# Kernel tuning notes

Hardware: AMD Instinct MI355X
Metric: run time of the kernel (lower is better)

The kernel has to match this reference:

```python
import jax, jax.numpy as jnp
import numpy as np

H = 16      # num_head
D = 1024    # feat_dim
DK = D // H # per-head dim
B, S = 2, 2048


def setup_inputs() -> dict:
    key = jax.random.key(0)
    ks = jax.random.split(key, 11)
    scale = 1.0 / np.sqrt(D)
    inp = {
        'query': jax.random.normal(ks[0], (B, S, D), jnp.float32),
        'key':   jax.random.normal(ks[1], (B, S, D), jnp.float32),
        'value': jax.random.normal(ks[2], (B, S, D), jnp.float32),
        # causal lower-triangular mask (seq, seq); 0 entries get -1e9
        'mask':  jnp.tril(jnp.ones((S, S), jnp.int32)),
        # torch nn.Linear params: y = x @ W.T + b
        'w_q': jax.random.normal(ks[3], (D, D), jnp.float32) * scale,
        'b_q': jax.random.normal(ks[4], (D,), jnp.float32) * scale,
        'w_k': jax.random.normal(ks[5], (D, D), jnp.float32) * scale,
        'b_k': jax.random.normal(ks[6], (D,), jnp.float32) * scale,
        'w_v': jax.random.normal(ks[7], (D, D), jnp.float32) * scale,
        'b_v': jax.random.normal(ks[8], (D,), jnp.float32) * scale,
        'w_out': jax.random.normal(ks[9], (D, D), jnp.float32) * scale,
        'b_out': jax.random.normal(ks[10], (D,), jnp.float32) * scale,
    }
    return inp


def reference(query, key, value, mask, w_q, b_q, w_k, b_k, w_v, b_v, w_out, b_out):
    b = query.shape[0]
    # projections + split heads -> (b, h, s, d_k)
    def proj(x, w, bias):
        y = x @ w.T + bias
        return y.reshape(b, -1, H, DK).transpose(0, 2, 1, 3)
    q = proj(query, w_q, b_q)
    k = proj(key, w_k, b_k)
    v = proj(value, w_v, b_v)
    # scaled dot-product attention with materialized score matrix
    scores = jnp.einsum('bhqd,bhkd->bhqk', q, k) / np.sqrt(DK).astype(jnp.float32)
    scores = jnp.where(mask == 0, jnp.float32(-1e9), scores)
    attn = jax.nn.softmax(scores, axis=-1)  # dropout is identity in eval mode
    x = jnp.einsum('bhqk,bhkd->bhqd', attn, v)
    x = x.transpose(0, 2, 1, 3).reshape(b, -1, H * DK)
    return x @ w_out.T + b_out
```

## Files before the change

### kernel.cpp

```cpp
#include <hip/hip_runtime.h>

typedef unsigned short u16;
typedef __attribute__((ext_vector_type(8))) short short8;
typedef __attribute__((ext_vector_type(8))) unsigned short u16x8;
typedef __attribute__((ext_vector_type(4))) float floatx4;

#define S2LOG 0.18033688f

__device__ __forceinline__ u16 f2bf(float f) {
    unsigned int u = __float_as_uint(f);
    return (u16)((u + 0x7FFFu + ((u >> 16) & 1u)) >> 16);
}
__device__ __forceinline__ u16 f2bf_hu(float f) {
    return (u16)((__float_as_uint(f) + 0x8000u) >> 16);
}
__device__ __forceinline__ void gl_lds16(const u16* g, u16* l) {
    __builtin_amdgcn_global_load_lds(
        (const __attribute__((address_space(1))) void*)g,
        (__attribute__((address_space(3))) void*)l, 16, 0, 0);
}

__global__ __launch_bounds__(256) void cvt_all(
    const float* __restrict__ q, const float* __restrict__ k, const float* __restrict__ v,
    const float* __restrict__ wq, const float* __restrict__ wk,
    const float* __restrict__ wv, const float* __restrict__ wo,
    u16* __restrict__ ws)
{
    const int b = blockIdx.x, t = threadIdx.x;
    const float* src; u16* dst; long blk;
    if      (b < 2048) { src = q;  dst = ws;            blk = b; }
    else if (b < 4096) { src = k;  dst = ws + 4194304;  blk = b - 2048; }
    else if (b < 6144) { src = v;  dst = ws + 8388608;  blk = b - 4096; }
    else if (b < 6656) { src = wq; dst = ws + 12582912; blk = b - 6144; }
    else if (b < 7168) { src = wk; dst = ws + 13631488; blk = b - 6656; }
    else if (b < 7680) { src = wv; dst = ws + 14680064; blk = b - 7168; }
    else               { src = wo; dst = ws + 15728640; blk = b - 7680; }
    const long i = blk * 2048 + (long)t * 8;
    const float4 a = *(const float4*)(src + i);
    const float4 c = *(const float4*)(src + i + 4);
    u16x8 o;
    o[0] = f2bf(a.x); o[1] = f2bf(a.y); o[2] = f2bf(a.z); o[3] = f2bf(a.w);
    o[4] = f2bf(c.x); o[5] = f2bf(c.y); o[6] = f2bf(c.z); o[7] = f2bf(c.w);
    *(u16x8*)(dst + i) = o;
}

__device__ __forceinline__ void gemm_core64(
    const u16* __restrict__ A, const u16* __restrict__ Bw,
    int m0, int n0, floatx4 (&acc)[2][4])
{
    __shared__ u16 As[2][128 * 64];
    __shared__ u16 Bs[2][64 * 64];
    const int t = threadIdx.x, w = t >> 6;
    const int lane = t & 63, col = lane & 15, quad = lane >> 4;
    const int c7 = col & 7;

#pragma unroll
    for (int i = 0; i < 2; ++i)
#pragma unroll
        for (int j = 0; j < 4; ++j) acc[i][j] = (floatx4)0.f;

    auto stage = [&](int k0, int buf) {
#pragma unroll
        for (int jj = 0; jj < 4; ++jj) {
            const int c = jj * 256 + t;
            const int row = c >> 3, kc = (c & 7) ^ (row & 7);
            gl_lds16(A + (size_t)(m0 + row) * 1024 + k0 + kc * 8,
                     As[buf] + (jj * 256 + w * 64) * 8);
        }
#pragma unroll
        for (int jj = 0; jj < 2; ++jj) {
            const int c = jj * 256 + t;
            const int row = c >> 3, kc = (c & 7) ^ (row & 7);
            gl_lds16(Bw + (size_t)(n0 + row) * 1024 + k0 + kc * 8,
                     Bs[buf] + (jj * 256 + w * 64) * 8);
        }
    };

    stage(0, 0);
    int cur = 0;
    for (int k0 = 0; k0 < 1024; k0 += 64) {
        asm volatile("s_waitcnt vmcnt(0)" ::: "memory");
        __builtin_amdgcn_s_barrier();
        if (k0 + 64 < 1024) stage(k0 + 64, cur ^ 1);
#pragma unroll
        for (int ks = 0; ks < 2; ++ks) {
            const int swz = (ks * 4 + quad) ^ c7;
            short8 af[2], bf[4];
#pragma unroll
            for (int i = 0; i < 2; ++i)
                af[i] = *(const short8*)&As[cur][((w * 32 + i * 16 + col) * 8 + swz) * 8];
#pragma unroll
            for (int j = 0; j < 4; ++j)
                bf[j] = *(const short8*)&Bs[cur][((j * 16 + col) * 8 + swz) * 8];
#pragma unroll
            for (int i = 0; i < 2; ++i)
#pragma unroll
                for (int j = 0; j < 4; ++j)
                    acc[i][j] = __builtin_amdgcn_mfma_f32_16x16x32_bf16(
                        af[i], bf[j], acc[i][j], 0, 0, 0);
        }
        asm volatile("s_waitcnt lgkmcnt(0)" ::: "memory");
        cur ^= 1;
    }
}

__device__ __forceinline__ void gemm_core128(
    const u16* __restrict__ A, const u16* __restrict__ Bw,
    int m0, int n0, floatx4 (&acc)[4][4])
{
    __shared__ u16 As[2][128 * 64];
    __shared__ u16 Bs[2][128 * 64];
    const int t = threadIdx.x, w = t >> 6;
    const int lane = t & 63, col = lane & 15, quad = lane >> 4;
    const int c7 = col & 7;
    const int wr = (w >> 1) * 64, wc = (w & 1) * 64;

#pragma unroll
    for (int i = 0; i < 4; ++i)
#pragma unroll
        for (int j = 0; j < 4; ++j) acc[i][j] = (floatx4)0.f;

    auto stage = [&](int k0, int buf) {
#pragma unroll
        for (int jj = 0; jj < 4; ++jj) {
            const int c = jj * 256 + t;
            const int row = c >> 3, kc = (c & 7) ^ (row & 7);
            gl_lds16(A + (size_t)(m0 + row) * 1024 + k0 + kc * 8,
                     As[buf] + (jj * 256 + w * 64) * 8);
            gl_lds16(Bw + (size_t)(n0 + row) * 1024 + k0 + kc * 8,
                     Bs[buf] + (jj * 256 + w * 64) * 8);
        }
    };

    stage(0, 0);
    int cur = 0;
    for (int k0 = 0; k0 < 1024; k0 += 64) {
        asm volatile("s_waitcnt vmcnt(0)" ::: "memory");
        __builtin_amdgcn_s_barrier();
        if (k0 + 64 < 1024) stage(k0 + 64, cur ^ 1);
#pragma unroll
        for (int ks = 0; ks < 2; ++ks) {
            const int swz = (ks * 4 + quad) ^ c7;
            short8 af[4], bf[4];
#pragma unroll
            for (int i = 0; i < 4; ++i)
                af[i] = *(const short8*)&As[cur][((wr + i * 16 + col) * 8 + swz) * 8];
#pragma unroll
            for (int j = 0; j < 4; ++j)
                bf[j] = *(const short8*)&Bs[cur][((wc + j * 16 + col) * 8 + swz) * 8];
#pragma unroll
            for (int i = 0; i < 4; ++i)
#pragma unroll
                for (int j = 0; j < 4; ++j)
                    acc[i][j] = __builtin_amdgcn_mfma_f32_16x16x32_bf16(
                        af[i], bf[j], acc[i][j], 0, 0, 0);
        }
        asm volatile("s_waitcnt lgkmcnt(0)" ::: "memory");
        cur ^= 1;
    }
}

__global__ __launch_bounds__(256) void gemm_qkv(
    const u16* __restrict__ xq, const u16* __restrict__ xk, const u16* __restrict__ xv,
    const u16* __restrict__ wqb, const u16* __restrict__ wkb, const u16* __restrict__ wvb,
    const float* __restrict__ bq, const float* __restrict__ bk, const float* __restrict__ bv,
    u16* __restrict__ Qh, u16* __restrict__ Kh, u16* __restrict__ Vt)
{
    const int z = blockIdx.z;
    const u16*   A    = z == 0 ? xq  : z == 1 ? xk  : xv;
    const u16*   Bw   = z == 0 ? wqb : z == 1 ? wkb : wvb;
    const float* bias = z == 0 ? bq  : z == 1 ? bk  : bv;
    u16*         out  = z == 0 ? Qh  : z == 1 ? Kh  : Vt;
    const float  scale = z == 0 ? S2LOG : 1.0f;
    const int m0 = blockIdx.x * 128, n0 = blockIdx.y * 128;

    floatx4 acc[4][4];
    gemm_core128(A, Bw, m0, n0, acc);

    const int t = threadIdx.x, w = t >> 6;
    const int lane = t & 63, col = lane & 15, quad = lane >> 4;
    const int wr = (w >> 1) * 64, wc = (w & 1) * 64;
#pragma unroll
    for (int i = 0; i < 4; ++i)
#pragma unroll
        for (int j = 0; j < 4; ++j)
#pragma unroll
            for (int reg = 0; reg < 4; ++reg) {
                const int gm = m0 + wr + i * 16 + quad * 4 + reg;
                const int gn = n0 + wc + j * 16 + col;
                const float val = (acc[i][j][reg] + bias[gn]) * scale;
                const int bb = gm >> 11, ss = gm & 2047, hh = gn >> 6, dd = gn & 63;
                if (z != 2)
                    out[(((size_t)bb * 16 + hh) * 2048 + ss) * 64 + dd] = f2bf(val);
                else
                    out[(((size_t)bb * 16 + hh) * 64 + dd) * 2048 + ss] = f2bf(val);
            }
}

__global__ __launch_bounds__(256) void gemm_out(
    const u16* __restrict__ A, const u16* __restrict__ Bw,
    const float* __restrict__ bias, float* __restrict__ out)
{
    const int m0 = blockIdx.x * 128, n0 = blockIdx.y * 64;
    floatx4 acc[2][4];
    gemm_core64(A, Bw, m0, n0, acc);
    const int t = threadIdx.x, w = t >> 6;
    const int lane = t & 63, col = lane & 15, quad = lane >> 4;
#pragma unroll
    for (int i = 0; i < 2; ++i)
#pragma unroll
        for (int j = 0; j < 4; ++j)
#pragma unroll
            for (int reg = 0; reg < 4; ++reg) {
                const int gm = m0 + w * 32 + i * 16 + quad * 4 + reg;
                const int gn = n0 + j * 16 + col;
                out[(size_t)gm * 1024 + gn] = acc[i][j][reg] + bias[gn];
            }
}

__global__ __launch_bounds__(256) void attn_mfma(
    const u16* __restrict__ Qh, const u16* __restrict__ Kh,
    const u16* __restrict__ Vt, u16* __restrict__ ctx)
{
    __shared__ u16 QPs[64 * 64];
    __shared__ u16 Ks[2][64 * 64];
    __shared__ u16 Vs[2][64 * 64];
    const int t = threadIdx.x, w = t >> 6;
    const int lane = t & 63, col = lane & 15, quad = lane >> 4;
    const int c7 = col & 7;
    const int bh = blockIdx.y;
    const int qt = (bh < 16) ? (31 - (int)blockIdx.x) : (int)blockIdx.x;
    const int q0 = qt * 64;
    const u16* qg = Qh + ((size_t)bh * 2048 + q0) * 64;
    const u16* kg = Kh + (size_t)bh * 2048 * 64;
    const u16* vg = Vt + (size_t)bh * 2048 * 64;

    auto stage = [&](int tile, int buf) {
#pragma unroll
        for (int jj = 0; jj < 2; ++jj) {
            const int c = jj * 256 + t;
            const int row = c >> 3, kc = (c & 7) ^ (row & 7);
            gl_lds16(kg + (size_t)(tile * 64 + row) * 64 + kc * 8,
                     Ks[buf] + (jj * 256 + w * 64) * 8);
            gl_lds16(vg + (size_t)row * 2048 + tile * 64 + kc * 8,
                     Vs[buf] + (jj * 256 + w * 64) * 8);
        }
    };

#pragma unroll
    for (int jj = 0; jj < 2; ++jj) {
        const int c = jj * 256 + t;
        const int row = c >> 3, kc = (c & 7) ^ (row & 7);
        gl_lds16(qg + (size_t)row * 64 + kc * 8, QPs + (jj * 256 + w * 64) * 8);
    }
    stage(0, 0);
    asm volatile("s_waitcnt vmcnt(4)" ::: "memory");
    __builtin_amdgcn_s_barrier();

    short8 qf[2];
#pragma unroll
    for (int ks = 0; ks < 2; ++ks)
        qf[ks] = *(const short8*)
            &QPs[((w * 16 + col) * 8 + ((ks * 4 + quad) ^ c7)) * 8];
    asm volatile("s_waitcnt lgkmcnt(0)" ::: "memory");
    __builtin_amdgcn_s_barrier();

    floatx4 oacc[4], lacc;
    lacc = (floatx4)0.f;
#pragma unroll
    for (int j = 0; j < 4; ++j) oacc[j] = (floatx4)0.f;
    short8 ones;
#pragma unroll
    for (int i = 0; i < 8; ++i) ones[i] = (short)0x3F80;

    const int ktmax = qt;
    int cur = 0;
    for (int kt = 0; kt <= ktmax; ++kt) {
        asm volatile("s_waitcnt vmcnt(0)" ::: "memory");
        __builtin_amdgcn_s_barrier();
        if (kt + 1 <= ktmax) stage(kt + 1, cur ^ 1);

        floatx4 sa[4];
#pragma unroll
        for (int j = 0; j < 4; ++j) sa[j] = (floatx4)0.f;
#pragma unroll
        for (int ks = 0; ks < 2; ++ks) {
            const int swz = (ks * 4 + quad) ^ c7;
            short8 kf[4];
#pragma unroll
            for (int jc = 0; jc < 4; ++jc)
                kf[jc] = *(const short8*)&Ks[cur][((jc * 16 + col) * 8 + swz) * 8];
            __builtin_amdgcn_s_setprio(1);
#pragma unroll
            for (int jc = 0; jc < 4; ++jc)
                sa[jc] = __builtin_amdgcn_mfma_f32_16x16x32_bf16(
                    qf[ks], kf[jc], sa[jc], 0, 0, 0);
            __builtin_amdgcn_s_setprio(0);
        }
        const bool pm = (kt == qt);
#pragma unroll
        for (int reg = 0; reg < 4; ++reg) {
            const int prow = w * 16 + quad * 4 + reg;
            const int qrow = q0 + prow;
            const int pr7 = prow & 7;
            u16* pr = &QPs[prow * 64 + (col & 7)];
#pragma unroll
            for (int jc = 0; jc < 4; ++jc) {
                float p = __builtin_amdgcn_exp2f(sa[jc][reg]);
                if (pm && (kt * 64 + jc * 16 + col > qrow)) p = 0.f;
                pr[((2 * jc + (col >> 3)) ^ pr7) << 3] = f2bf_hu(p);
            }
        }
#pragma unroll
        for (int ks = 0; ks < 2; ++ks) {
            const int swz = (ks * 4 + quad) ^ c7;
            short8 pf, vf[4];
            pf = *(const short8*)&QPs[((w * 16 + col) * 8 + swz) * 8];
#pragma unroll
            for (int jd = 0; jd < 4; ++jd)
                vf[jd] = *(const short8*)&Vs[cur][((jd * 16 + col) * 8 + swz) * 8];
            __builtin_amdgcn_s_setprio(1);
            lacc = __builtin_amdgcn_mfma_f32_16x16x32_bf16(pf, ones, lacc, 0, 0, 0);
#pragma unroll
            for (int jd = 0; jd < 4; ++jd)
                oacc[jd] = __builtin_amdgcn_mfma_f32_16x16x32_bf16(
                    pf, vf[jd], oacc[jd], 0, 0, 0);
            __builtin_amdgcn_s_setprio(0);
        }
        cur ^= 1;
    }

    const int bb = bh >> 4, hh = bh & 15;
#pragma unroll
    for (int reg = 0; reg < 4; ++reg) {
        const float inv = __builtin_amdgcn_rcpf(lacc[reg]);
        const int qrow = q0 + w * 16 + quad * 4 + reg;
#pragma unroll
        for (int jd = 0; jd < 4; ++jd)
            ctx[((size_t)bb * 2048 + qrow) * 1024 + hh * 64 + jd * 16 + col] =
                f2bf(oacc[jd][reg] * inv);
    }
}

extern "C" void kernel_launch(void* const* d_in, const int* in_sizes, int n_in,
                              void* d_out, int out_size, void* d_ws, size_t ws_size,
                              hipStream_t stream)
{
    const float* query = (const float*)d_in[0];
    const float* key   = (const float*)d_in[1];
    const float* value = (const float*)d_in[2];
    const float* w_q   = (const float*)d_in[4];
    const float* b_q   = (const float*)d_in[5];
    const float* w_k   = (const float*)d_in[6];
    const float* b_k   = (const float*)d_in[7];
    const float* w_v   = (const float*)d_in[8];
    const float* b_v   = (const float*)d_in[9];
    const float* w_out = (const float*)d_in[10];
    const float* b_out = (const float*)d_in[11];

    u16* W = (u16*)d_ws;
    u16* xq  = W;
    u16* xk  = W + 4194304;
    u16* xv  = W + 8388608;
    u16* wqb = W + 12582912;
    u16* wkb = W + 13631488;
    u16* wvb = W + 14680064;
    u16* wob = W + 15728640;
    u16* Qh  = W + 16777216;
    u16* Kh  = W + 20971520;
    u16* Vtw = W + 25165824;
    u16* ctx = W + 29360128;

    hipLaunchKernelGGL(cvt_all, dim3(8192), dim3(256), 0, stream,
                       query, key, value, w_q, w_k, w_v, w_out, W);

    hipLaunchKernelGGL(gemm_qkv, dim3(32, 8, 3), dim3(256), 0, stream,
                       xq, xk, xv, wqb, wkb, wvb, b_q, b_k, b_v, Qh, Kh, Vtw);

    hipLaunchKernelGGL(attn_mfma, dim3(32, 32), dim3(256), 0, stream, Qh, Kh, Vtw, ctx);

    hipLaunchKernelGGL(gemm_out, dim3(32, 16), dim3(256), 0, stream,
                       ctx, wob, b_out, (float*)d_out);
}
```

Measured before the change: 244.7 us.

## Load K/V MFMA fragments directly from global memory instead of LDS staging

The attention kernel no longer stages Q, K and V tiles through double-buffered LDS with async global-to-LDS copies and barriers. Each wave now reads its MFMA operand fragments straight from global memory (relying on L2/L1 reuse across waves), and LDS is kept only for the P tile. The intent is to remove barriers and LDS traffic and shrink the LDS footprint, and launch bounds now ask for 3 blocks per CU for more occupancy. The cost is four-fold redundant global loads across the waves, no explicit prefetch of the next tile, and exposed load latency inside the loop.

Result: slower. 333.7 us (+36.4%).

```diff
diff --git a/kernel.cpp b/kernel.cpp
--- a/kernel.cpp
+++ b/kernel.cpp
@@ -218,13 +218,11 @@
             }
 }
 
-__global__ __launch_bounds__(256) void attn_mfma(
+__global__ __launch_bounds__(256, 3) void attn_mfma(
     const u16* __restrict__ Qh, const u16* __restrict__ Kh,
     const u16* __restrict__ Vt, u16* __restrict__ ctx)
 {
-    __shared__ u16 QPs[64 * 64];
-    __shared__ u16 Ks[2][64 * 64];
-    __shared__ u16 Vs[2][64 * 64];
+    __shared__ u16 Ps[64 * 64];
     const int t = threadIdx.x, w = t >> 6;
     const int lane = t & 63, col = lane & 15, quad = lane >> 4;
     const int c7 = col & 7;
@@ -235,35 +233,10 @@
     const u16* kg = Kh + (size_t)bh * 2048 * 64;
     const u16* vg = Vt + (size_t)bh * 2048 * 64;
 
-    auto stage = [&](int tile, int buf) {
-#pragma unroll
-        for (int jj = 0; jj < 2; ++jj) {
-            const int c = jj * 256 + t;
-            const int row = c >> 3, kc = (c & 7) ^ (row & 7);
-            gl_lds16(kg + (size_t)(tile * 64 + row) * 64 + kc * 8,
-                     Ks[buf] + (jj * 256 + w * 64) * 8);
-            gl_lds16(vg + (size_t)row * 2048 + tile * 64 + kc * 8,
-                     Vs[buf] + (jj * 256 + w * 64) * 8);
-        }
-    };
-
-#pragma unroll
-    for (int jj = 0; jj < 2; ++jj) {
-        const int c = jj * 256 + t;
-        const int row = c >> 3, kc = (c & 7) ^ (row & 7);
-        gl_lds16(qg + (size_t)row * 64 + kc * 8, QPs + (jj * 256 + w * 64) * 8);
-    }
-    stage(0, 0);
-    asm volatile("s_waitcnt vmcnt(4)" ::: "memory");
-    __builtin_amdgcn_s_barrier();
-
     short8 qf[2];
 #pragma unroll
     for (int ks = 0; ks < 2; ++ks)
-        qf[ks] = *(const short8*)
-            &QPs[((w * 16 + col) * 8 + ((ks * 4 + quad) ^ c7)) * 8];
-    asm volatile("s_waitcnt lgkmcnt(0)" ::: "memory");
-    __builtin_amdgcn_s_barrier();
+        qf[ks] = *(const short8*)(qg + (size_t)(w * 16 + col) * 64 + (ks * 4 + quad) * 8);
 
     floatx4 oacc[4], lacc;
     lacc = (floatx4)0.f;
@@ -273,37 +246,44 @@
 #pragma unroll
     for (int i = 0; i < 8; ++i) ones[i] = (short)0x3F80;
 
+    const u16* kb = kg + (size_t)col * 64 + quad * 8;
+    const u16* vb = vg + (size_t)col * 2048 + quad * 8;
+
     const int ktmax = qt;
-    int cur = 0;
     for (int kt = 0; kt <= ktmax; ++kt) {
-        asm volatile("s_waitcnt vmcnt(0)" ::: "memory");
-        __builtin_amdgcn_s_barrier();
-        if (kt + 1 <= ktmax) stage(kt + 1, cur ^ 1);
+        short8 kf[2][4];
+#pragma unroll
+        for (int ks = 0; ks < 2; ++ks)
+#pragma unroll
+            for (int jc = 0; jc < 4; ++jc)
+                kf[ks][jc] = *(const short8*)(kb + (size_t)kt * 4096 + jc * 1024 + ks * 32);
 
         floatx4 sa[4];
 #pragma unroll
         for (int j = 0; j < 4; ++j) sa[j] = (floatx4)0.f;
-#pragma unroll
-        for (int ks = 0; ks < 2; ++ks) {
-            const int swz = (ks * 4 + quad) ^ c7;
-            short8 kf[4];
-#pragma unroll
-            for (int jc = 0; jc < 4; ++jc)
-                kf[jc] = *(const short8*)&Ks[cur][((jc * 16 + col) * 8 + swz) * 8];
-            __builtin_amdgcn_s_setprio(1);
+        __builtin_amdgcn_s_setprio(1);
+#pragma unroll
+        for (int ks = 0; ks < 2; ++ks)
 #pragma unroll
             for (int jc = 0; jc < 4; ++jc)
                 sa[jc] = __builtin_amdgcn_mfma_f32_16x16x32_bf16(
-                    qf[ks], kf[jc], sa[jc], 0, 0, 0);
-            __builtin_amdgcn_s_setprio(0);
-        }
+                    qf[ks], kf[ks][jc], sa[jc], 0, 0, 0);
+        __builtin_amdgcn_s_setprio(0);
+
+        short8 vf[2][4];
+#pragma unroll
+        for (int ks = 0; ks < 2; ++ks)
+#pragma unroll
+            for (int jd = 0; jd < 4; ++jd)
+                vf[ks][jd] = *(const short8*)(vb + (size_t)jd * 32768 + kt * 64 + ks * 32);
+
         const bool pm = (kt == qt);
 #pragma unroll
         for (int reg = 0; reg < 4; ++reg) {
             const int prow = w * 16 + quad * 4 + reg;
             const int qrow = q0 + prow;
             const int pr7 = prow & 7;
-            u16* pr = &QPs[prow * 64 + (col & 7)];
+            u16* pr = &Ps[prow * 64 + (col & 7)];
 #pragma unroll
             for (int jc = 0; jc < 4; ++jc) {
                 float p = __builtin_amdgcn_exp2f(sa[jc][reg]);
@@ -314,20 +294,15 @@
 #pragma unroll
         for (int ks = 0; ks < 2; ++ks) {
             const int swz = (ks * 4 + quad) ^ c7;
-            short8 pf, vf[4];
-            pf = *(const short8*)&QPs[((w * 16 + col) * 8 + swz) * 8];
-#pragma unroll
-            for (int jd = 0; jd < 4; ++jd)
-                vf[jd] = *(const short8*)&Vs[cur][((jd * 16 + col) * 8 + swz) * 8];
+            short8 pf = *(const short8*)&Ps[((w * 16 + col) * 8 + swz) * 8];
             __builtin_amdgcn_s_setprio(1);
             lacc = __builtin_amdgcn_mfma_f32_16x16x32_bf16(pf, ones, lacc, 0, 0, 0);
 #pragma unroll
             for (int jd = 0; jd < 4; ++jd)
                 oacc[jd] = __builtin_amdgcn_mfma_f32_16x16x32_bf16(
-                    pf, vf[jd], oacc[jd], 0, 0, 0);
+                    pf, vf[ks][jd], oacc[jd], 0, 0, 0);
             __builtin_amdgcn_s_setprio(0);
         }
-        cur ^= 1;
     }
 
     const int bb = bh >> 4, hh = bh & 15;
```
